# Kernel optimization log

Measured on AMD Instinct MI355X. Metric: run time of the kernel, lower is better.

The kernel has to match this reference:

```python
import jax, jax.numpy as jnp
import numpy as np

N_NODES = 100000
N_EDGES = 2000000
F_IN = 64
HID = 64
N_MP = 6  # hidden message-passing layers


def setup_inputs() -> dict:
    key = jax.random.key(0)
    ks = jax.random.split(key, 8)
    x = jax.random.normal(ks[0], (N_NODES, F_IN), dtype=jnp.float32)
    edge_index = jax.random.randint(ks[1], (2, N_EDGES), 0, N_NODES, dtype=jnp.int64)
    # GCNConv params: weight [in, out], bias [out] (glorot-ish scale)
    def w(k, i, o):
        return jax.random.normal(k, (i, o), dtype=jnp.float32) * (1.0 / np.sqrt(i))
    W_i = w(ks[2], F_IN, HID)
    b_i = jnp.zeros((HID,), jnp.float32)
    W_h = jax.random.normal(ks[3], (N_MP, HID, HID), dtype=jnp.float32) * (1.0 / np.sqrt(HID))
    b_h = jnp.zeros((N_MP, HID), jnp.float32)
    W_o = w(ks[4], HID, 1)
    b_o = jnp.zeros((1,), jnp.float32)
    return {"x": x, "edge_index": edge_index, "W_i": W_i, "b_i": b_i,
            "W_h": W_h, "b_h": b_h, "W_o": W_o, "b_o": b_o}


def reference(x, edge_index, W_i, b_i, W_h, b_h, W_o, b_o):
    n = x.shape[0]
    loop = jnp.arange(n, dtype=edge_index.dtype)
    # add self loops (PyG GCNConv default)
    src = jnp.concatenate([edge_index[0], loop])  # [E+N]
    dst = jnp.concatenate([edge_index[1], loop])
    # symmetric normalization: deg computed over dst (col) with self loops
    deg = jax.ops.segment_sum(jnp.ones(dst.shape, x.dtype), dst, num_segments=n)
    dinv = jax.lax.rsqrt(deg)  # deg >= 1 due to self loops
    norm = (dinv[src] * dinv[dst])[:, None]  # [E+N, 1]

    def conv(h, W, b):
        h = h @ W                                   # [N, out]
        msg = h[src] * norm                         # gather + scale  [E+N, out]
        return jax.ops.segment_sum(msg, dst, num_segments=n) + b

    h = jax.nn.relu(conv(x, W_i, b_i))
    for l in range(W_h.shape[0]):
        h = jax.nn.relu(conv(h, W_h[l], b_h[l]))
    return conv(h, W_o, b_o)  # [N, 1]
```

## Files before the change

kernel.cpp:

```cpp
#include <hip/hip_runtime.h>
#include <math.h>

#define TPB 256
#define BSH 8
#define BMAX 512
#define EPB 4096


__global__ __launch_bounds__(TPB) void k_hist(const int* __restrict__ dst,
                                              int* __restrict__ bucketCnt,
                                              int nE, int nbuck) {
  __shared__ int h[BMAX];
  for (int i = threadIdx.x; i < BMAX; i += TPB) h[i] = 0;
  __syncthreads();
  int base = blockIdx.x * EPB;
  for (int i = threadIdx.x; i < EPB; i += TPB) {
    int e = base + i;
    if (e < nE) atomicAdd(&h[dst[e] >> BSH], 1);
  }
  __syncthreads();
  for (int i = threadIdx.x; i < nbuck; i += TPB)
    if (h[i]) atomicAdd(&bucketCnt[i], h[i]);
}

__global__ __launch_bounds__(BMAX) void k_bscan(const int* __restrict__ bucketCnt,
                                                int* __restrict__ bOff,
                                                int* __restrict__ gCur,
                                                int* __restrict__ rowPtr,
                                                int nbuck, int n, int nE) {
  __shared__ int sd[BMAX];
  int t = threadIdx.x;
  int v = (t < nbuck) ? bucketCnt[t] : 0;
  sd[t] = v;
  __syncthreads();
  for (int off = 1; off < BMAX; off <<= 1) {
    int add = (t >= off) ? sd[t - off] : 0;
    __syncthreads();
    sd[t] += add;
    __syncthreads();
  }
  if (t < nbuck) {
    bOff[t + 1] = sd[t];
    gCur[t] = sd[t] - v;
  }
  if (t == 0) { bOff[0] = 0; rowPtr[n] = nE; }
}

__global__ __launch_bounds__(TPB) void k_bucket(const int* __restrict__ src,
                                                const int* __restrict__ dst,
                                                int* __restrict__ gCur,
                                                int* __restrict__ pairBuf,
                                                int nE, int nbuck) {
  __shared__ int   hist[BMAX];
  __shared__ int   baseL[BMAX];
  __shared__ int   sp[EPB];
  __shared__ short sbk[EPB];
  for (int i = threadIdx.x; i < BMAX; i += TPB) hist[i] = 0;
  __syncthreads();
  int cb = blockIdx.x * EPB;
  for (int i = threadIdx.x; i < EPB; i += TPB) {
    int e = cb + i;
    if (e < nE) {
      int s = src[e], d = dst[e];
      int b = d >> BSH;
      sp[i]  = s | ((d & ((1 << BSH) - 1)) << 20);
      sbk[i] = (short)b;
      atomicAdd(&hist[b], 1);
    } else sbk[i] = -1;
  }
  __syncthreads();
  for (int i = threadIdx.x; i < nbuck; i += TPB)
    baseL[i] = hist[i] ? atomicAdd(&gCur[i], hist[i]) : 0;
  __syncthreads();
  for (int i = threadIdx.x; i < BMAX; i += TPB) hist[i] = 0;
  __syncthreads();
  for (int i = threadIdx.x; i < EPB; i += TPB) {
    int b = sbk[i];
    if (b >= 0) {
      int r = atomicAdd(&hist[b], 1);
      pairBuf[baseL[b] + r] = sp[i];
    }
  }
}

__global__ __launch_bounds__(TPB) void k_final(const int* __restrict__ pairBuf,
                                               const int* __restrict__ bOff,
                                               int* __restrict__ rowPtr,
                                               int* __restrict__ col,
                                               float* __restrict__ dinv,
                                               int n) {
  __shared__ int h[TPB];
  __shared__ int ex[TPB];
  int t = threadIdx.x;
  int b = blockIdx.x;
  int p0 = bOff[b], p1 = bOff[b + 1];
  h[t] = 0;
  __syncthreads();
  for (int i = p0 + t; i < p1; i += TPB)
    atomicAdd(&h[pairBuf[i] >> 20], 1);
  __syncthreads();
  int v = h[t];
  ex[t] = v;
  __syncthreads();
  for (int off = 1; off < TPB; off <<= 1) {
    int add = (t >= off) ? ex[t - off] : 0;
    __syncthreads();
    ex[t] += add;
    __syncthreads();
  }
  int excl = ex[t] - v;
  int node = (b << BSH) + t;
  if (node < n) {
    rowPtr[node] = p0 + excl;
    dinv[node]   = rsqrtf((float)(v + 1));
  }
  __syncthreads();
  h[t] = excl;
  __syncthreads();
  for (int i = p0 + t; i < p1; i += TPB) {
    int p = pairBuf[i];
    int r = atomicAdd(&h[p >> 20], 1);
    col[p0 + r] = p & 0xFFFFF;
  }
}


__global__ __launch_bounds__(TPB, 4) void k_gemm(const float* __restrict__ H,
                                                 const float* __restrict__ W,
                                                 const float* __restrict__ dinv,
                                                 float* __restrict__ HWS,
                                                 int relu, int rows) {
  __shared__ float Wl[64 * 64];
  __shared__ float Hl[64][68];
  const int tid = threadIdx.x;
  const int c0 = (tid & 15) * 4;
  const int r0 = (tid >> 4) * 4;
  const int row0 = blockIdx.x * 64;

  for (int i = tid; i < 64 * 16; i += TPB)
    ((float4*)Wl)[i] = ((const float4*)W)[i];

  for (int i = tid; i < 64 * 16; i += TPB) {
    int r = i >> 4, q = i & 15;
    int gr = row0 + r;
    float4 v = make_float4(0.f, 0.f, 0.f, 0.f);
    if (gr < rows) v = ((const float4*)(H + (size_t)gr * 64))[q];
    if (relu) {
      v.x = fmaxf(v.x, 0.f); v.y = fmaxf(v.y, 0.f);
      v.z = fmaxf(v.z, 0.f); v.w = fmaxf(v.w, 0.f);
    }
    *(float4*)&Hl[r][q * 4] = v;
  }
  __syncthreads();

  float acc[4][4] = {{0.f,0.f,0.f,0.f},{0.f,0.f,0.f,0.f},
                     {0.f,0.f,0.f,0.f},{0.f,0.f,0.f,0.f}};
#pragma unroll 4
  for (int k = 0; k < 64; ++k) {
    float4 w = *(const float4*)&Wl[k * 64 + c0];
    float h0 = Hl[r0 + 0][k];
    float h1 = Hl[r0 + 1][k];
    float h2 = Hl[r0 + 2][k];
    float h3 = Hl[r0 + 3][k];
    acc[0][0] = fmaf(h0, w.x, acc[0][0]); acc[0][1] = fmaf(h0, w.y, acc[0][1]);
    acc[0][2] = fmaf(h0, w.z, acc[0][2]); acc[0][3] = fmaf(h0, w.w, acc[0][3]);
    acc[1][0] = fmaf(h1, w.x, acc[1][0]); acc[1][1] = fmaf(h1, w.y, acc[1][1]);
    acc[1][2] = fmaf(h1, w.z, acc[1][2]); acc[1][3] = fmaf(h1, w.w, acc[1][3]);
    acc[2][0] = fmaf(h2, w.x, acc[2][0]); acc[2][1] = fmaf(h2, w.y, acc[2][1]);
    acc[2][2] = fmaf(h2, w.z, acc[2][2]); acc[2][3] = fmaf(h2, w.w, acc[2][3]);
    acc[3][0] = fmaf(h3, w.x, acc[3][0]); acc[3][1] = fmaf(h3, w.y, acc[3][1]);
    acc[3][2] = fmaf(h3, w.z, acc[3][2]); acc[3][3] = fmaf(h3, w.w, acc[3][3]);
  }

#pragma unroll
  for (int i = 0; i < 4; ++i) {
    int gr = row0 + r0 + i;
    if (gr < rows) {
      float s = dinv[gr];
      float4 o = make_float4(acc[i][0] * s, acc[i][1] * s,
                             acc[i][2] * s, acc[i][3] * s);
      *(float4*)&HWS[(size_t)gr * 64 + c0] = o;
    }
  }
}

__global__ __launch_bounds__(TPB) void k_scatter(const float* __restrict__ HWS,
                                                 const int* __restrict__ rowPtr,
                                                 const int* __restrict__ col,
                                                 const float* __restrict__ dinv,
                                                 const float* __restrict__ bias,
                                                 float* __restrict__ OUT, int n) {
  int wave = blockIdx.x * (TPB / 64) + (threadIdx.x >> 6);
  int lane = threadIdx.x & 63;
  if (wave >= n) return;
  const int node = wave;
  float acc = HWS[node * 64 + lane];
  int e0 = rowPtr[node], e1 = rowPtr[node + 1];
  int deg = e1 - e0;
  for (int base = 0; base < deg; base += 64) {
    int m = deg - base; if (m > 64) m = 64;
    int idxv = (lane < m) ? col[e0 + base + lane] : 0;
    int j = 0;
    for (; j + 8 <= m; j += 8) {
      int s0 = __shfl(idxv, j,     64);
      int s1 = __shfl(idxv, j + 1, 64);
      int s2 = __shfl(idxv, j + 2, 64);
      int s3 = __shfl(idxv, j + 3, 64);
      int s4 = __shfl(idxv, j + 4, 64);
      int s5 = __shfl(idxv, j + 5, 64);
      int s6 = __shfl(idxv, j + 6, 64);
      int s7 = __shfl(idxv, j + 7, 64);
      float v0 = HWS[s0 * 64 + lane];
      float v1 = HWS[s1 * 64 + lane];
      float v2 = HWS[s2 * 64 + lane];
      float v3 = HWS[s3 * 64 + lane];
      float v4 = HWS[s4 * 64 + lane];
      float v5 = HWS[s5 * 64 + lane];
      float v6 = HWS[s6 * 64 + lane];
      float v7 = HWS[s7 * 64 + lane];
      acc += ((v0 + v1) + (v2 + v3)) + ((v4 + v5) + (v6 + v7));
    }
    for (; j + 4 <= m; j += 4) {
      int s0 = __shfl(idxv, j,     64);
      int s1 = __shfl(idxv, j + 1, 64);
      int s2 = __shfl(idxv, j + 2, 64);
      int s3 = __shfl(idxv, j + 3, 64);
      float v0 = HWS[s0 * 64 + lane];
      float v1 = HWS[s1 * 64 + lane];
      float v2 = HWS[s2 * 64 + lane];
      float v3 = HWS[s3 * 64 + lane];
      acc += (v0 + v1) + (v2 + v3);
    }
    for (; j < m; ++j) {
      int s = __shfl(idxv, j, 64);
      acc += HWS[s * 64 + lane];
    }
  }
  OUT[node * 64 + lane] = dinv[node] * acc + bias[lane];
}

__global__ __launch_bounds__(TPB) void k_fdot(const float* __restrict__ H,
                                              const float* __restrict__ Wo,
                                              const float* __restrict__ dinv,
                                              float* __restrict__ hws1, int n) {
  int i = blockIdx.x * TPB + threadIdx.x;
  if (i >= n) return;
  const float4* Hv = (const float4*)(H + (size_t)i * 64);
  float acc = 0.f;
#pragma unroll
  for (int q = 0; q < 16; ++q) {
    float4 v = Hv[q];
    acc += fmaxf(v.x, 0.f) * Wo[4 * q + 0];
    acc += fmaxf(v.y, 0.f) * Wo[4 * q + 1];
    acc += fmaxf(v.z, 0.f) * Wo[4 * q + 2];
    acc += fmaxf(v.w, 0.f) * Wo[4 * q + 3];
  }
  hws1[i] = acc * dinv[i];
}

__global__ __launch_bounds__(TPB) void k_fscat(const float* __restrict__ hws1,
                                               const int* __restrict__ rowPtr,
                                               const int* __restrict__ col,
                                               const float* __restrict__ dinv,
                                               const float* __restrict__ bo,
                                               float* __restrict__ out, int n) {
  int i = blockIdx.x * TPB + threadIdx.x;
  if (i >= n) return;
  float acc = hws1[i];
  int e0 = rowPtr[i], e1 = rowPtr[i + 1];
  for (int e = e0; e < e1; ++e) acc += hws1[col[e]];
  out[i] = dinv[i] * acc + bo[0];
}


extern "C" void kernel_launch(void* const* d_in, const int* in_sizes, int n_in,
                              void* d_out, int out_size, void* d_ws, size_t ws_size,
                              hipStream_t stream) {
  const float* x   = (const float*)d_in[0];
  const int*   ei  = (const int*)d_in[1];
  const float* W_i = (const float*)d_in[2];
  const float* b_i = (const float*)d_in[3];
  const float* W_h = (const float*)d_in[4];
  const float* b_h = (const float*)d_in[5];
  const float* W_o = (const float*)d_in[6];
  const float* b_o = (const float*)d_in[7];

  const int N = in_sizes[0] / 64;
  const int E = in_sizes[1] / 2;
  const int* srcArr = ei;
  const int* dstArr = ei + E;
  const int nbuck = (N + (1 << BSH) - 1) >> BSH;

  char* w = (char*)d_ws;
  auto take = [&](size_t bytes) -> char* {
    char* p = w;
    w += (bytes + 255) & ~(size_t)255;
    return p;
  };
  int*   rowPtr    = (int*)take((size_t)(N + 1) * 4);
  int*   col       = (int*)take((size_t)E * 4);
  float* dinv      = (float*)take((size_t)N * 4);
  int*   bucketCnt = (int*)take((size_t)BMAX * 4);
  int*   bOff      = (int*)take((size_t)(BMAX + 1) * 4);
  int*   gCur      = (int*)take((size_t)BMAX * 4);
  float* bufH      = (float*)take((size_t)N * 64 * 4);
  float* bufS      = (float*)take((size_t)N * 64 * 4);
  float* hws1      = (float*)take((size_t)N * 4);
  int*   pairBuf   = (int*)bufS;
  (void)ws_size; (void)n_in; (void)out_size;

  const int nbN    = (N + TPB - 1) / TPB;
  const int nbEd   = (E + EPB - 1) / EPB;
  const int nbGemm = (N + 63) / 64;
  const int nbScat = (N + 3) / 4;

  hipMemsetAsync(bucketCnt, 0, (size_t)BMAX * 4, stream);
  k_hist  <<<nbEd, TPB, 0, stream>>>(dstArr, bucketCnt, E, nbuck);
  k_bscan <<<1, BMAX, 0, stream>>>(bucketCnt, bOff, gCur, rowPtr, nbuck, N, E);
  k_bucket<<<nbEd, TPB, 0, stream>>>(srcArr, dstArr, gCur, pairBuf, E, nbuck);
  k_final <<<nbuck, TPB, 0, stream>>>(pairBuf, bOff, rowPtr, col, dinv, N);

  k_gemm   <<<nbGemm, TPB, 0, stream>>>(x, W_i, dinv, bufS, 0, N);
  k_scatter<<<nbScat, TPB, 0, stream>>>(bufS, rowPtr, col, dinv, b_i, bufH, N);

  for (int l = 0; l < 6; ++l) {
    k_gemm   <<<nbGemm, TPB, 0, stream>>>(bufH, W_h + (size_t)l * 64 * 64, dinv, bufS, 1, N);
    k_scatter<<<nbScat, TPB, 0, stream>>>(bufS, rowPtr, col, dinv, b_h + (size_t)l * 64, bufH, N);
  }

  k_fdot <<<nbN, TPB, 0, stream>>>(bufH, W_o, dinv, hws1, N);
  k_fscat<<<nbN, TPB, 0, stream>>>(hws1, rowPtr, col, dinv, b_o, (float*)d_out, N);
}
```

Before: 724.1 us.

## Slice features into 8-wide column panels for cache-local neighbor aggregation

Stores the intermediate node features as eight separate column slices, each holding 8 floats per node (32 bytes per row). The gather-scatter kernel now works on one slice per block, so the table being randomly gathered is about 3.2 MB per slice instead of the full 25.6 MB. The aim is for the random neighbor reads to hit L2/LLC. In exchange, each edge index is read 8 times and each gather is only 32 bytes wide. The change also halves the CSR bucket size to 128 nodes, giving more final-stage blocks, and unrolls the final scalar aggregation into 4 accumulators.

```diff
diff --git a/kernel.cpp b/kernel.cpp
--- a/kernel.cpp
+++ b/kernel.cpp
@@ -2,8 +2,9 @@
 #include <math.h>
 
 #define TPB 256
-#define BSH 8
-#define BMAX 512
+#define BSH 7
+#define NPB (1 << BSH)
+#define BMAX 1024
 #define EPB 4096
 
 
@@ -63,7 +64,7 @@
     if (e < nE) {
       int s = src[e], d = dst[e];
       int b = d >> BSH;
-      sp[i]  = s | ((d & ((1 << BSH) - 1)) << 20);
+      sp[i]  = s | ((d & (NPB - 1)) << 20);
       sbk[i] = (short)b;
       atomicAdd(&hist[b], 1);
     } else sbk[i] = -1;
@@ -89,33 +90,35 @@
                                                int* __restrict__ col,
                                                float* __restrict__ dinv,
                                                int n) {
-  __shared__ int h[TPB];
-  __shared__ int ex[TPB];
+  __shared__ int h[NPB];
+  __shared__ int ex[NPB];
   int t = threadIdx.x;
   int b = blockIdx.x;
   int p0 = bOff[b], p1 = bOff[b + 1];
-  h[t] = 0;
+  if (t < NPB) h[t] = 0;
   __syncthreads();
   for (int i = p0 + t; i < p1; i += TPB)
     atomicAdd(&h[pairBuf[i] >> 20], 1);
   __syncthreads();
-  int v = h[t];
-  ex[t] = v;
-  __syncthreads();
-  for (int off = 1; off < TPB; off <<= 1) {
-    int add = (t >= off) ? ex[t - off] : 0;
+  int v = 0;
+  if (t < NPB) { v = h[t]; ex[t] = v; }
+  __syncthreads();
+  for (int off = 1; off < NPB; off <<= 1) {
+    int add = 0;
+    if (t < NPB && t >= off) add = ex[t - off];
     __syncthreads();
-    ex[t] += add;
+    if (t < NPB) ex[t] += add;
     __syncthreads();
   }
-  int excl = ex[t] - v;
-  int node = (b << BSH) + t;
-  if (node < n) {
-    rowPtr[node] = p0 + excl;
-    dinv[node]   = rsqrtf((float)(v + 1));
-  }
-  __syncthreads();
-  h[t] = excl;
+  if (t < NPB) {
+    int node = (b << BSH) + t;
+    if (node < n) {
+      int excl = ex[t] - v;
+      rowPtr[node] = p0 + excl;
+      dinv[node]   = rsqrtf((float)(v + 1));
+      h[t] = excl;
+    }
+  }
   __syncthreads();
   for (int i = p0 + t; i < p1; i += TPB) {
     int p = pairBuf[i];
@@ -129,7 +132,8 @@
                                                  const float* __restrict__ W,
                                                  const float* __restrict__ dinv,
                                                  float* __restrict__ HWS,
-                                                 int relu, int rows) {
+                                                 int relu, int denseIn,
+                                                 int rows, int N8) {
   __shared__ float Wl[64 * 64];
   __shared__ float Hl[64][68];
   const int tid = threadIdx.x;
@@ -140,16 +144,31 @@
   for (int i = tid; i < 64 * 16; i += TPB)
     ((float4*)Wl)[i] = ((const float4*)W)[i];
 
-  for (int i = tid; i < 64 * 16; i += TPB) {
-    int r = i >> 4, q = i & 15;
-    int gr = row0 + r;
-    float4 v = make_float4(0.f, 0.f, 0.f, 0.f);
-    if (gr < rows) v = ((const float4*)(H + (size_t)gr * 64))[q];
-    if (relu) {
-      v.x = fmaxf(v.x, 0.f); v.y = fmaxf(v.y, 0.f);
-      v.z = fmaxf(v.z, 0.f); v.w = fmaxf(v.w, 0.f);
-    }
-    *(float4*)&Hl[r][q * 4] = v;
+  if (denseIn) {
+    for (int i = tid; i < 64 * 16; i += TPB) {
+      int r = i >> 4, q = i & 15;
+      int gr = row0 + r;
+      float4 v = make_float4(0.f, 0.f, 0.f, 0.f);
+      if (gr < rows) v = ((const float4*)(H + (size_t)gr * 64))[q];
+      if (relu) {
+        v.x = fmaxf(v.x, 0.f); v.y = fmaxf(v.y, 0.f);
+        v.z = fmaxf(v.z, 0.f); v.w = fmaxf(v.w, 0.f);
+      }
+      *(float4*)&Hl[r][q * 4] = v;
+    }
+  } else {
+    for (int i = tid; i < 64 * 16; i += TPB) {
+      int s = i >> 7, j = i & 127, r = j >> 1, half = j & 1;
+      int gr = row0 + r;
+      float4 v = make_float4(0.f, 0.f, 0.f, 0.f);
+      if (gr < rows)
+        v = *(const float4*)&H[(size_t)s * N8 + (size_t)gr * 8 + half * 4];
+      if (relu) {
+        v.x = fmaxf(v.x, 0.f); v.y = fmaxf(v.y, 0.f);
+        v.z = fmaxf(v.z, 0.f); v.w = fmaxf(v.w, 0.f);
+      }
+      *(float4*)&Hl[r][s * 8 + half * 4] = v;
+    }
   }
   __syncthreads();
 
@@ -172,6 +191,8 @@
     acc[3][2] = fmaf(h3, w.z, acc[3][2]); acc[3][3] = fmaf(h3, w.w, acc[3][3]);
   }
 
+  const int sOut = (tid & 15) >> 1;
+  const int cc   = (tid & 1) * 4;
 #pragma unroll
   for (int i = 0; i < 4; ++i) {
     int gr = row0 + r0 + i;
@@ -179,81 +200,77 @@
       float s = dinv[gr];
       float4 o = make_float4(acc[i][0] * s, acc[i][1] * s,
                              acc[i][2] * s, acc[i][3] * s);
-      *(float4*)&HWS[(size_t)gr * 64 + c0] = o;
-    }
-  }
-}
-
-__global__ __launch_bounds__(TPB) void k_scatter(const float* __restrict__ HWS,
-                                                 const int* __restrict__ rowPtr,
-                                                 const int* __restrict__ col,
-                                                 const float* __restrict__ dinv,
-                                                 const float* __restrict__ bias,
-                                                 float* __restrict__ OUT, int n) {
-  int wave = blockIdx.x * (TPB / 64) + (threadIdx.x >> 6);
-  int lane = threadIdx.x & 63;
-  if (wave >= n) return;
-  const int node = wave;
-  float acc = HWS[node * 64 + lane];
-  int e0 = rowPtr[node], e1 = rowPtr[node + 1];
-  int deg = e1 - e0;
-  for (int base = 0; base < deg; base += 64) {
-    int m = deg - base; if (m > 64) m = 64;
-    int idxv = (lane < m) ? col[e0 + base + lane] : 0;
-    int j = 0;
-    for (; j + 8 <= m; j += 8) {
-      int s0 = __shfl(idxv, j,     64);
-      int s1 = __shfl(idxv, j + 1, 64);
-      int s2 = __shfl(idxv, j + 2, 64);
-      int s3 = __shfl(idxv, j + 3, 64);
-      int s4 = __shfl(idxv, j + 4, 64);
-      int s5 = __shfl(idxv, j + 5, 64);
-      int s6 = __shfl(idxv, j + 6, 64);
-      int s7 = __shfl(idxv, j + 7, 64);
-      float v0 = HWS[s0 * 64 + lane];
-      float v1 = HWS[s1 * 64 + lane];
-      float v2 = HWS[s2 * 64 + lane];
-      float v3 = HWS[s3 * 64 + lane];
-      float v4 = HWS[s4 * 64 + lane];
-      float v5 = HWS[s5 * 64 + lane];
-      float v6 = HWS[s6 * 64 + lane];
-      float v7 = HWS[s7 * 64 + lane];
-      acc += ((v0 + v1) + (v2 + v3)) + ((v4 + v5) + (v6 + v7));
-    }
-    for (; j + 4 <= m; j += 4) {
-      int s0 = __shfl(idxv, j,     64);
-      int s1 = __shfl(idxv, j + 1, 64);
-      int s2 = __shfl(idxv, j + 2, 64);
-      int s3 = __shfl(idxv, j + 3, 64);
-      float v0 = HWS[s0 * 64 + lane];
-      float v1 = HWS[s1 * 64 + lane];
-      float v2 = HWS[s2 * 64 + lane];
-      float v3 = HWS[s3 * 64 + lane];
-      acc += (v0 + v1) + (v2 + v3);
-    }
-    for (; j < m; ++j) {
-      int s = __shfl(idxv, j, 64);
-      acc += HWS[s * 64 + lane];
-    }
-  }
-  OUT[node * 64 + lane] = dinv[node] * acc + bias[lane];
+      *(float4*)&HWS[(size_t)sOut * N8 + (size_t)gr * 8 + cc] = o;
+    }
+  }
+}
+
+__global__ __launch_bounds__(TPB) void k_scat8(const float* __restrict__ HWS,
+                                               const int* __restrict__ rowPtr,
+                                               const int* __restrict__ col,
+                                               const float* __restrict__ dinv,
+                                               const float* __restrict__ bias,
+                                               float* __restrict__ OUT,
+                                               int n, int N8) {
+  const int slice = blockIdx.x & 7;
+  const int grp   = blockIdx.x >> 3;
+  const int t     = threadIdx.x;
+  const int node  = grp * 32 + (t >> 3);
+  const int c     = t & 7;
+  if (node >= n) return;
+
+  const float* __restrict__ tab = HWS + (size_t)slice * N8;
+  float acc = tab[(size_t)node * 8 + c];
+
+  const int e1 = rowPtr[node + 1];
+  int e = rowPtr[node];
+  for (; e + 8 <= e1; e += 8) {
+    int i0 = col[e],     i1 = col[e + 1], i2 = col[e + 2], i3 = col[e + 3];
+    int i4 = col[e + 4], i5 = col[e + 5], i6 = col[e + 6], i7 = col[e + 7];
+    float v0 = tab[(size_t)i0 * 8 + c];
+    float v1 = tab[(size_t)i1 * 8 + c];
+    float v2 = tab[(size_t)i2 * 8 + c];
+    float v3 = tab[(size_t)i3 * 8 + c];
+    float v4 = tab[(size_t)i4 * 8 + c];
+    float v5 = tab[(size_t)i5 * 8 + c];
+    float v6 = tab[(size_t)i6 * 8 + c];
+    float v7 = tab[(size_t)i7 * 8 + c];
+    acc += ((v0 + v1) + (v2 + v3)) + ((v4 + v5) + (v6 + v7));
+  }
+  for (; e + 4 <= e1; e += 4) {
+    int i0 = col[e], i1 = col[e + 1], i2 = col[e + 2], i3 = col[e + 3];
+    float v0 = tab[(size_t)i0 * 8 + c];
+    float v1 = tab[(size_t)i1 * 8 + c];
+    float v2 = tab[(size_t)i2 * 8 + c];
+    float v3 = tab[(size_t)i3 * 8 + c];
+    acc += (v0 + v1) + (v2 + v3);
+  }
+  for (; e < e1; ++e) acc += tab[(size_t)col[e] * 8 + c];
+
+  OUT[(size_t)slice * N8 + (size_t)node * 8 + c] =
+      dinv[node] * acc + bias[slice * 8 + c];
 }
 
 __global__ __launch_bounds__(TPB) void k_fdot(const float* __restrict__ H,
                                               const float* __restrict__ Wo,
                                               const float* __restrict__ dinv,
-                                              float* __restrict__ hws1, int n) {
+                                              float* __restrict__ hws1,
+                                              int n, int N8) {
   int i = blockIdx.x * TPB + threadIdx.x;
   if (i >= n) return;
-  const float4* Hv = (const float4*)(H + (size_t)i * 64);
   float acc = 0.f;
 #pragma unroll
-  for (int q = 0; q < 16; ++q) {
-    float4 v = Hv[q];
-    acc += fmaxf(v.x, 0.f) * Wo[4 * q + 0];
-    acc += fmaxf(v.y, 0.f) * Wo[4 * q + 1];
-    acc += fmaxf(v.z, 0.f) * Wo[4 * q + 2];
-    acc += fmaxf(v.w, 0.f) * Wo[4 * q + 3];
+  for (int s = 0; s < 8; ++s) {
+    float4 a = *(const float4*)&H[(size_t)s * N8 + (size_t)i * 8];
+    float4 b = *(const float4*)&H[(size_t)s * N8 + (size_t)i * 8 + 4];
+    acc += fmaxf(a.x, 0.f) * Wo[s * 8 + 0];
+    acc += fmaxf(a.y, 0.f) * Wo[s * 8 + 1];
+    acc += fmaxf(a.z, 0.f) * Wo[s * 8 + 2];
+    acc += fmaxf(a.w, 0.f) * Wo[s * 8 + 3];
+    acc += fmaxf(b.x, 0.f) * Wo[s * 8 + 4];
+    acc += fmaxf(b.y, 0.f) * Wo[s * 8 + 5];
+    acc += fmaxf(b.z, 0.f) * Wo[s * 8 + 6];
+    acc += fmaxf(b.w, 0.f) * Wo[s * 8 + 7];
   }
   hws1[i] = acc * dinv[i];
 }
@@ -266,10 +283,17 @@
                                                float* __restrict__ out, int n) {
   int i = blockIdx.x * TPB + threadIdx.x;
   if (i >= n) return;
-  float acc = hws1[i];
+  float a0 = hws1[i], a1 = 0.f, a2 = 0.f, a3 = 0.f;
   int e0 = rowPtr[i], e1 = rowPtr[i + 1];
-  for (int e = e0; e < e1; ++e) acc += hws1[col[e]];
-  out[i] = dinv[i] * acc + bo[0];
+  int e = e0;
+  for (; e + 4 <= e1; e += 4) {
+    a0 += hws1[col[e]];
+    a1 += hws1[col[e + 1]];
+    a2 += hws1[col[e + 2]];
+    a3 += hws1[col[e + 3]];
+  }
+  for (; e < e1; ++e) a0 += hws1[col[e]];
+  out[i] = dinv[i] * ((a0 + a1) + (a2 + a3)) + bo[0];
 }
 
 
@@ -287,9 +311,10 @@
 
   const int N = in_sizes[0] / 64;
   const int E = in_sizes[1] / 2;
+  const int N8 = N * 8;
   const int* srcArr = ei;
   const int* dstArr = ei + E;
-  const int nbuck = (N + (1 << BSH) - 1) >> BSH;
+  const int nbuck = (N + NPB - 1) >> BSH;
 
   char* w = (char*)d_ws;
   auto take = [&](size_t bytes) -> char* {
@@ -312,7 +337,7 @@
   const int nbN    = (N + TPB - 1) / TPB;
   const int nbEd   = (E + EPB - 1) / EPB;
   const int nbGemm = (N + 63) / 64;
-  const int nbScat = (N + 3) / 4;
+  const int nbScat = 8 * ((N + 31) / 32);
 
   hipMemsetAsync(bucketCnt, 0, (size_t)BMAX * 4, stream);
   k_hist  <<<nbEd, TPB, 0, stream>>>(dstArr, bucketCnt, E, nbuck);
@@ -320,14 +345,14 @@
   k_bucket<<<nbEd, TPB, 0, stream>>>(srcArr, dstArr, gCur, pairBuf, E, nbuck);
   k_final <<<nbuck, TPB, 0, stream>>>(pairBuf, bOff, rowPtr, col, dinv, N);
 
-  k_gemm   <<<nbGemm, TPB, 0, stream>>>(x, W_i, dinv, bufS, 0, N);
-  k_scatter<<<nbScat, TPB, 0, stream>>>(bufS, rowPtr, col, dinv, b_i, bufH, N);
+  k_gemm <<<nbGemm, TPB, 0, stream>>>(x, W_i, dinv, bufS, 0, 1, N, N8);
+  k_scat8<<<nbScat, TPB, 0, stream>>>(bufS, rowPtr, col, dinv, b_i, bufH, N, N8);
 
   for (int l = 0; l < 6; ++l) {
-    k_gemm   <<<nbGemm, TPB, 0, stream>>>(bufH, W_h + (size_t)l * 64 * 64, dinv, bufS, 1, N);
-    k_scatter<<<nbScat, TPB, 0, stream>>>(bufS, rowPtr, col, dinv, b_h + (size_t)l * 64, bufH, N);
-  }
-
-  k_fdot <<<nbN, TPB, 0, stream>>>(bufH, W_o, dinv, hws1, N);
+    k_gemm <<<nbGemm, TPB, 0, stream>>>(bufH, W_h + (size_t)l * 64 * 64, dinv, bufS, 1, 0, N, N8);
+    k_scat8<<<nbScat, TPB, 0, stream>>>(bufS, rowPtr, col, dinv, b_h + (size_t)l * 64, bufH, N, N8);
+  }
+
+  k_fdot <<<nbN, TPB, 0, stream>>>(bufH, W_o, dinv, hws1, N, N8);
   k_fscat<<<nbN, TPB, 0, stream>>>(hws1, rowPtr, col, dinv, b_o, (float*)d_out, N);
 }
```

Result: slower. 879.4 us (+21.4%).
